# Kernel optimization log

Hardware: AMD Instinct MI355X
Metric: run time of the kernel (lower is better)

## Reference

```python
import jax, jax.numpy as jnp
import numpy as np


def _gcn_layer(x, W, b, src, dst, norm, n_nodes):
    # x: [N, Fin]; transform first (PyG GCNConv): h = x @ W
    h = x @ W  # [N, Fout]
    # gather-scale-scatter: out[d] += norm_e * h[s] over edges (incl. self loops)
    msgs = h[src] * norm[:, None]  # [E+N, Fout]
    agg = jax.ops.segment_sum(msgs, dst, num_segments=n_nodes)
    return agg + b


def setup_inputs() -> dict:
    key = jax.random.key(0)
    k1, k2, k3, k4 = jax.random.split(key, 4)
    N, E, F_IN, HID, OUT = 50000, 800000, 128, 256, 128
    x = jax.random.normal(k1, (N, F_IN), dtype=jnp.float32)
    edge_index = jax.random.randint(k2, (2, E), 0, N, dtype=jnp.int64)
    W1 = jax.random.normal(k3, (F_IN, HID), dtype=jnp.float32) / np.sqrt(F_IN)
    b1 = jnp.zeros((HID,), dtype=jnp.float32)
    W2 = jax.random.normal(k4, (HID, OUT), dtype=jnp.float32) / np.sqrt(HID)
    b2 = jnp.zeros((OUT,), dtype=jnp.float32)
    return {"x": x, "edge_index": edge_index, "W1": W1, "b1": b1, "W2": W2, "b2": b2}


def reference(x, edge_index, W1, b1, W2, b2):
    N = x.shape[0]
    # GCN normalization with self loops: A_hat = D^-1/2 (A + I) D^-1/2
    self_loops = jnp.arange(N, dtype=edge_index.dtype)
    src = jnp.concatenate([edge_index[0], self_loops])
    dst = jnp.concatenate([edge_index[1], self_loops])
    deg = jax.ops.segment_sum(jnp.ones_like(dst, dtype=x.dtype), dst, num_segments=N)
    dinv = jnp.where(deg > 0, jax.lax.rsqrt(deg), 0.0)
    norm = dinv[src] * dinv[dst]  # [E+N]
    h = _gcn_layer(x, W1, b1, src, dst, norm, N)
    h = jax.nn.relu(h)  # dropout is identity in eval mode
    out = _gcn_layer(h, W2, b2, src, dst, norm, N)
    return out  # unsupervised mode returns raw embeddings [N, 128]
```

## Files before the change

kernel.cpp:

```cpp
#include <hip/hip_runtime.h>
#include <hip/hip_bf16.h>


static constexpr int N_NODES = 50000;
static constexpr int N_EDGES = 800000;
static constexpr int F_IN = 128;
static constexpr int HID  = 256;
static constexpr int F_OUT = 128;

typedef __attribute__((ext_vector_type(8))) short short8;
typedef __attribute__((ext_vector_type(4))) float f32x4;

__device__ __forceinline__ unsigned short f2bf(float f) {
    union { float f; unsigned u; } x; x.f = f;
    unsigned r = x.u + 0x7FFF + ((x.u >> 16) & 1);
    return (unsigned short)(r >> 16);
}
__device__ __forceinline__ float bf2f(unsigned short h) {
    union { unsigned u; float f; } x; x.u = ((unsigned)h) << 16;
    return x.f;
}

__global__ void deg_pos_kernel(const int* __restrict__ dst, int* __restrict__ deg,
                               int* __restrict__ pos, int E) {
    int i = blockIdx.x * blockDim.x + threadIdx.x;
    if (i < E) pos[i] = atomicAdd(&deg[dst[i]], 1);
}

__global__ __launch_bounds__(256) void scan_reduce_dinv(const int* __restrict__ deg,
                                                        int* __restrict__ bsums,
                                                        float* __restrict__ dinv, int N) {
    int i = blockIdx.x * 256 + threadIdx.x;
    int v = (i < N) ? deg[i] : 0;
    if (i < N) dinv[i] = rsqrtf((float)(v + 1));
#pragma unroll
    for (int ofs = 32; ofs > 0; ofs >>= 1) v += __shfl_down(v, ofs);
    __shared__ int ws[4];
    if ((threadIdx.x & 63) == 0) ws[threadIdx.x >> 6] = v;
    __syncthreads();
    if (threadIdx.x == 0) bsums[blockIdx.x] = ws[0] + ws[1] + ws[2] + ws[3];
}

__global__ __launch_bounds__(256) void scan_final(const int* __restrict__ deg,
                                                  const int* __restrict__ bsums,
                                                  int* __restrict__ off, int N, int nb) {
    __shared__ int bs[256];
    __shared__ int s[256];
    const int tid = threadIdx.x;
    bs[tid] = (tid < nb) ? bsums[tid] : 0;
    const int i = blockIdx.x * 256 + tid;
    int v = (i < N) ? deg[i] : 0;
    s[tid] = v;
    __syncthreads();
    for (int ofs = 1; ofs < 256; ofs <<= 1) {
        int tb = (tid >= ofs) ? bs[tid - ofs] : 0;
        int tv = (tid >= ofs) ? s[tid - ofs] : 0;
        __syncthreads();
        bs[tid] += tb;
        s[tid] += tv;
        __syncthreads();
    }
    int bbase = (blockIdx.x == 0) ? 0 : bs[blockIdx.x - 1];
    int excl = (tid == 0) ? 0 : s[tid - 1];
    if (i <= N) off[i] = bbase + excl;
}

__global__ void scatter_kernel(const int* __restrict__ src, const int* __restrict__ dst,
                               const int* __restrict__ pos, const int* __restrict__ off,
                               int* __restrict__ csr, int E) {
    int i = blockIdx.x * blockDim.x + threadIdx.x;
    if (i < E) csr[off[dst[i]] + pos[i]] = src[i];
}

__global__ void prep_kernel(const float* __restrict__ x, const float* __restrict__ dinv,
                            unsigned short* __restrict__ xs,
                            const float* __restrict__ W1, unsigned short* __restrict__ w1t,
                            const float* __restrict__ W2, unsigned short* __restrict__ w2t,
                            int NBX, int NB1) {
    const int b = blockIdx.x;
    if (b < NBX) {
        int i = b * 256 + threadIdx.x;
        if (i < N_NODES * F_IN / 8) {
            float dv = dinv[i >> 4];
            float4 v0 = ((const float4*)x)[i * 2];
            float4 v1 = ((const float4*)x)[i * 2 + 1];
            short8 o;
            o[0] = (short)f2bf(v0.x * dv); o[1] = (short)f2bf(v0.y * dv);
            o[2] = (short)f2bf(v0.z * dv); o[3] = (short)f2bf(v0.w * dv);
            o[4] = (short)f2bf(v1.x * dv); o[5] = (short)f2bf(v1.y * dv);
            o[6] = (short)f2bf(v1.z * dv); o[7] = (short)f2bf(v1.w * dv);
            *(short8*)(xs + (size_t)i * 8) = o;
        }
    } else if (b < NBX + NB1) {
        int t = (b - NBX) * 256 + threadIdx.x;
        if (t < F_IN * HID) {
            int n = t / F_IN, k = t - n * F_IN;
            w1t[t] = f2bf(W1[(size_t)k * HID + n]);
        }
    } else {
        int t = (b - NBX - NB1) * 256 + threadIdx.x;
        if (t < HID * F_OUT) {
            int n = t / HID, k = t - n * HID;
            w2t[t] = f2bf(W2[(size_t)k * F_OUT + n]);
        }
    }
}

template <int MODE>
__global__ __launch_bounds__(256) void agg_bf16(const unsigned short* __restrict__ hs,
                                                const int* __restrict__ off,
                                                const int* __restrict__ csr,
                                                const float* __restrict__ dinv,
                                                const float* __restrict__ bias,
                                                void* __restrict__ outp, int N) {
    const int wid = threadIdx.x >> 6;
    const int n = blockIdx.x * 4 + wid;
    if (n >= N) return;
    const int lane = threadIdx.x & 63;
    const int lane16 = lane & 15;
    const int slot = lane >> 4;

    float va[8], vb[8], vc[8], vd[8];
#pragma unroll
    for (int j = 0; j < 8; j++) { va[j] = 0.f; vb[j] = 0.f; vc[j] = 0.f; vd[j] = 0.f; }

    if (slot == 0) {
        short8 s = *(const short8*)(hs + (size_t)n * 128 + lane16 * 8);
#pragma unroll
        for (int j = 0; j < 8; j++) va[j] = bf2f((unsigned short)s[j]);
    }

    const int e0 = off[n];
    const int e1 = off[n + 1];
    for (int e = e0 + slot; e < e1; e += 16) {
        const int i1 = e + 4, i2 = e + 8, i3 = e + 12;
        const float f1 = (i1 < e1) ? 1.f : 0.f;
        const float f2 = (i2 < e1) ? 1.f : 0.f;
        const float f3 = (i3 < e1) ? 1.f : 0.f;
        const int c1 = min(i1, e1 - 1), c2 = min(i2, e1 - 1), c3 = min(i3, e1 - 1);
        int s0 = csr[e];
        int s1 = csr[c1];
        int s2 = csr[c2];
        int s3 = csr[c3];
        short8 v0 = *(const short8*)(hs + (size_t)s0 * 128 + lane16 * 8);
        short8 v1 = *(const short8*)(hs + (size_t)s1 * 128 + lane16 * 8);
        short8 v2 = *(const short8*)(hs + (size_t)s2 * 128 + lane16 * 8);
        short8 v3 = *(const short8*)(hs + (size_t)s3 * 128 + lane16 * 8);
#pragma unroll
        for (int j = 0; j < 8; j++) va[j] += bf2f((unsigned short)v0[j]);
#pragma unroll
        for (int j = 0; j < 8; j++) vb[j] = fmaf(f1, bf2f((unsigned short)v1[j]), vb[j]);
#pragma unroll
        for (int j = 0; j < 8; j++) vc[j] = fmaf(f2, bf2f((unsigned short)v2[j]), vc[j]);
#pragma unroll
        for (int j = 0; j < 8; j++) vd[j] = fmaf(f3, bf2f((unsigned short)v3[j]), vd[j]);
    }
#pragma unroll
    for (int j = 0; j < 8; j++) va[j] += vb[j] + vc[j] + vd[j];

#pragma unroll
    for (int j = 0; j < 8; j++) va[j] += __shfl_down(va[j], 32);
#pragma unroll
    for (int j = 0; j < 8; j++) va[j] += __shfl_down(va[j], 16);

    if (lane < 16) {
        float dv = dinv[n];
        if (MODE == 0) {
            short8 o;
#pragma unroll
            for (int j = 0; j < 8; j++) o[j] = (short)f2bf(va[j] * dv);
            *(short8*)((unsigned short*)outp + (size_t)n * 128 + lane * 8) = o;
        } else {
            float* op = (float*)outp + (size_t)n * 128 + lane * 8;
            float4 o0, o1;
            o0.x = va[0] * dv + bias[lane * 8 + 0];
            o0.y = va[1] * dv + bias[lane * 8 + 1];
            o0.z = va[2] * dv + bias[lane * 8 + 2];
            o0.w = va[3] * dv + bias[lane * 8 + 3];
            o1.x = va[4] * dv + bias[lane * 8 + 4];
            o1.y = va[5] * dv + bias[lane * 8 + 5];
            o1.z = va[6] * dv + bias[lane * 8 + 6];
            o1.w = va[7] * dv + bias[lane * 8 + 7];
            ((float4*)op)[0] = o0;
            ((float4*)op)[1] = o1;
        }
    }
}

template <int K, int NC, int EPI>
__global__ __launch_bounds__(256) void mfma_gemm(const unsigned short* __restrict__ X,
                                                 const unsigned short* __restrict__ WT,
                                                 const float* __restrict__ bias,
                                                 const float* __restrict__ dinv,
                                                 unsigned short* __restrict__ out, int M) {
    constexpr int KC = K / 32;
    constexpr int TILES = NC / 32;
    const int wid = threadIdx.x >> 6;
    const int lane = threadIdx.x & 63;
    const int an = lane & 15;
    const int q = lane >> 4;
    const int rowgrp = wid & 1;
    const int colgrp = wid >> 1;
    const int m0 = blockIdx.x * 64 + rowgrp * 32;
    const int ntbase = colgrp * TILES;

    short8 a[2][KC];
#pragma unroll
    for (int r = 0; r < 2; r++) {
        int row = m0 + r * 16 + an;
        if (row >= M) row = M - 1;
        const unsigned short* xp = X + (size_t)row * K + q * 8;
#pragma unroll
        for (int c = 0; c < KC; c++) a[r][c] = *(const short8*)(xp + c * 32);
    }

    auto do_tile = [&](int t) {
        const int col = (ntbase + t) * 16 + an;
        const unsigned short* wp = WT + (size_t)col * K + q * 8;
        short8 b[KC];
#pragma unroll
        for (int c = 0; c < KC; c++) b[c] = *(const short8*)(wp + c * 32);
        f32x4 acc0 = {0.f, 0.f, 0.f, 0.f};
        f32x4 acc1 = {0.f, 0.f, 0.f, 0.f};
#pragma unroll
        for (int c = 0; c < KC; c++) {
            acc0 = __builtin_amdgcn_mfma_f32_16x16x32_bf16(a[0][c], b[c], acc0, 0, 0, 0);
            acc1 = __builtin_amdgcn_mfma_f32_16x16x32_bf16(a[1][c], b[c], acc1, 0, 0, 0);
        }
        float bv = (EPI == 1) ? bias[col] : 0.f;
#pragma unroll
        for (int rr = 0; rr < 4; rr++) {
            int m = m0 + q * 4 + rr;
            if (m < M) {
                float v = acc0[rr];
                if (EPI == 1) v = fmaxf(v + bv, 0.f);
                else v *= dinv[m];
                out[(size_t)m * NC + col] = f2bf(v);
            }
            int m2 = m0 + 16 + q * 4 + rr;
            if (m2 < M) {
                float v = acc1[rr];
                if (EPI == 1) v = fmaxf(v + bv, 0.f);
                else v *= dinv[m2];
                out[(size_t)m2 * NC + col] = f2bf(v);
            }
        }
    };

    if constexpr (K == 128) {
#pragma unroll 4
        for (int t = 0; t < TILES; t++) do_tile(t);
    } else {
#pragma unroll 2
        for (int t = 0; t < TILES; t++) do_tile(t);
    }
}

extern "C" void kernel_launch(void* const* d_in, const int* in_sizes, int n_in,
                              void* d_out, int out_size, void* d_ws, size_t ws_size,
                              hipStream_t stream) {
    const float* x  = (const float*)d_in[0];
    const int*   ei = (const int*)d_in[1];
    const float* W1 = (const float*)d_in[2];
    const float* b1 = (const float*)d_in[3];
    const float* W2 = (const float*)d_in[4];
    const float* b2 = (const float*)d_in[5];

    const int N = N_NODES;
    const int E = N_EDGES;
    const int* srcp = ei;
    const int* dstp = ei + E;

    char* base = (char*)d_ws;
    size_t o = 0;
    auto alloc = [&](size_t bytes) {
        void* p = base + o;
        o = (o + bytes + 255) & ~(size_t)255;
        return p;
    };
    int*            deg  = (int*)alloc((size_t)N * 4);
    int*            offs = (int*)alloc((size_t)(N + 1) * 4);
    float*          dinv = (float*)alloc((size_t)N * 4);
    int*            bsum = (int*)alloc(256 * 4);
    int*            pos  = (int*)alloc((size_t)E * 4);
    int*            csr  = (int*)alloc((size_t)E * 4);
    unsigned short* xs   = (unsigned short*)alloc((size_t)N * F_IN * 2);
    unsigned short* Y    = (unsigned short*)alloc((size_t)N * F_IN * 2);
    unsigned short* h2   = (unsigned short*)alloc((size_t)N * HID * 2);
    unsigned short* w1t  = (unsigned short*)alloc((size_t)F_IN * HID * 2);
    unsigned short* w2t  = (unsigned short*)alloc((size_t)HID * F_OUT * 2);
    unsigned short* hs2  = xs;

    hipMemsetAsync(deg, 0, (size_t)N * 4, stream);

    const int NB = (N + 256) / 256;
    const int NBX = (N * F_IN / 8 + 255) / 256;
    const int NB1 = (F_IN * HID + 255) / 256;
    const int NB2 = (HID * F_OUT + 255) / 256;

    deg_pos_kernel<<<(E + 255) / 256, 256, 0, stream>>>(dstp, deg, pos, E);
    scan_reduce_dinv<<<NB, 256, 0, stream>>>(deg, bsum, dinv, N);
    scan_final<<<NB, 256, 0, stream>>>(deg, bsum, offs, N, NB);
    scatter_kernel<<<(E + 255) / 256, 256, 0, stream>>>(srcp, dstp, pos, offs, csr, E);
    prep_kernel<<<NBX + NB1 + NB2, 256, 0, stream>>>(x, dinv, xs, W1, w1t, W2, w2t, NBX, NB1);

    agg_bf16<0><<<(N + 3) / 4, 256, 0, stream>>>(xs, offs, csr, dinv, nullptr, Y, N);
    mfma_gemm<F_IN, HID, 1><<<(N + 63) / 64, 256, 0, stream>>>(Y, w1t, b1, nullptr, h2, N);

    mfma_gemm<HID, F_OUT, 0><<<(N + 63) / 64, 256, 0, stream>>>(h2, w2t, nullptr, dinv, hs2, N);
    agg_bf16<1><<<(N + 3) / 4, 256, 0, stream>>>(hs2, offs, csr, dinv, b2, d_out, N);
}
```

Measured before the change: 263.6 us.

## Fuse both GEMMs via LDS-resident hidden tile and merge prep into other kernels

After: 251.6 us. -4.5%, faster.

```diff
diff --git a/kernel.cpp b/kernel.cpp
--- a/kernel.cpp
+++ b/kernel.cpp
@@ -7,6 +7,7 @@
 static constexpr int F_IN = 128;
 static constexpr int HID  = 256;
 static constexpr int F_OUT = 128;
+static constexpr int H2P  = HID + 8;
 
 typedef __attribute__((ext_vector_type(8))) short short8;
 typedef __attribute__((ext_vector_type(4))) float f32x4;
@@ -21,10 +22,28 @@
     return x.f;
 }
 
-__global__ void deg_pos_kernel(const int* __restrict__ dst, int* __restrict__ deg,
-                               int* __restrict__ pos, int E) {
-    int i = blockIdx.x * blockDim.x + threadIdx.x;
-    if (i < E) pos[i] = atomicAdd(&deg[dst[i]], 1);
+__global__ void deg_wt_kernel(const int* __restrict__ dst, int* __restrict__ deg,
+                              int* __restrict__ pos, int E,
+                              const float* __restrict__ W1, unsigned short* __restrict__ w1t,
+                              const float* __restrict__ W2, unsigned short* __restrict__ w2t,
+                              int EB, int NB1) {
+    const int b = blockIdx.x;
+    if (b < EB) {
+        int i = b * 256 + threadIdx.x;
+        if (i < E) pos[i] = atomicAdd(&deg[dst[i]], 1);
+    } else if (b < EB + NB1) {
+        int t = (b - EB) * 256 + threadIdx.x;
+        if (t < F_IN * HID) {
+            int n = t / F_IN, k = t - n * F_IN;
+            w1t[t] = f2bf(W1[(size_t)k * HID + n]);
+        }
+    } else {
+        int t = (b - EB - NB1) * 256 + threadIdx.x;
+        if (t < HID * F_OUT) {
+            int n = t / HID, k = t - n * HID;
+            w2t[t] = f2bf(W2[(size_t)k * F_OUT + n]);
+        }
+    }
 }
 
 __global__ __launch_bounds__(256) void scan_reduce_dinv(const int* __restrict__ deg,
@@ -41,12 +60,30 @@
     if (threadIdx.x == 0) bsums[blockIdx.x] = ws[0] + ws[1] + ws[2] + ws[3];
 }
 
-__global__ __launch_bounds__(256) void scan_final(const int* __restrict__ deg,
-                                                  const int* __restrict__ bsums,
-                                                  int* __restrict__ off, int N, int nb) {
+__global__ __launch_bounds__(256) void scan_final_scalex(const int* __restrict__ deg,
+                                                         const int* __restrict__ bsums,
+                                                         int* __restrict__ off, int N, int nb,
+                                                         const float* __restrict__ x,
+                                                         const float* __restrict__ dinv,
+                                                         unsigned short* __restrict__ xs) {
+    const int tid = threadIdx.x;
+    if ((int)blockIdx.x >= nb) {
+        int i = (blockIdx.x - nb) * 256 + tid;
+        if (i < N_NODES * F_IN / 8) {
+            float dv = dinv[i >> 4];
+            float4 v0 = ((const float4*)x)[i * 2];
+            float4 v1 = ((const float4*)x)[i * 2 + 1];
+            short8 o;
+            o[0] = (short)f2bf(v0.x * dv); o[1] = (short)f2bf(v0.y * dv);
+            o[2] = (short)f2bf(v0.z * dv); o[3] = (short)f2bf(v0.w * dv);
+            o[4] = (short)f2bf(v1.x * dv); o[5] = (short)f2bf(v1.y * dv);
+            o[6] = (short)f2bf(v1.z * dv); o[7] = (short)f2bf(v1.w * dv);
+            *(short8*)(xs + (size_t)i * 8) = o;
+        }
+        return;
+    }
     __shared__ int bs[256];
     __shared__ int s[256];
-    const int tid = threadIdx.x;
     bs[tid] = (tid < nb) ? bsums[tid] : 0;
     const int i = blockIdx.x * 256 + tid;
     int v = (i < N) ? deg[i] : 0;
@@ -70,40 +107,6 @@
                                int* __restrict__ csr, int E) {
     int i = blockIdx.x * blockDim.x + threadIdx.x;
     if (i < E) csr[off[dst[i]] + pos[i]] = src[i];
-}
-
-__global__ void prep_kernel(const float* __restrict__ x, const float* __restrict__ dinv,
-                            unsigned short* __restrict__ xs,
-                            const float* __restrict__ W1, unsigned short* __restrict__ w1t,
-                            const float* __restrict__ W2, unsigned short* __restrict__ w2t,
-                            int NBX, int NB1) {
-    const int b = blockIdx.x;
-    if (b < NBX) {
-        int i = b * 256 + threadIdx.x;
-        if (i < N_NODES * F_IN / 8) {
-            float dv = dinv[i >> 4];
-            float4 v0 = ((const float4*)x)[i * 2];
-            float4 v1 = ((const float4*)x)[i * 2 + 1];
-            short8 o;
-            o[0] = (short)f2bf(v0.x * dv); o[1] = (short)f2bf(v0.y * dv);
-            o[2] = (short)f2bf(v0.z * dv); o[3] = (short)f2bf(v0.w * dv);
-            o[4] = (short)f2bf(v1.x * dv); o[5] = (short)f2bf(v1.y * dv);
-            o[6] = (short)f2bf(v1.z * dv); o[7] = (short)f2bf(v1.w * dv);
-            *(short8*)(xs + (size_t)i * 8) = o;
-        }
-    } else if (b < NBX + NB1) {
-        int t = (b - NBX) * 256 + threadIdx.x;
-        if (t < F_IN * HID) {
-            int n = t / F_IN, k = t - n * F_IN;
-            w1t[t] = f2bf(W1[(size_t)k * HID + n]);
-        }
-    } else {
-        int t = (b - NBX - NB1) * 256 + threadIdx.x;
-        if (t < HID * F_OUT) {
-            int n = t / HID, k = t - n * HID;
-            w2t[t] = f2bf(W2[(size_t)k * F_OUT + n]);
-        }
-    }
 }
 
 template <int MODE>
@@ -187,14 +190,14 @@
     }
 }
 
-template <int K, int NC, int EPI>
-__global__ __launch_bounds__(256) void mfma_gemm(const unsigned short* __restrict__ X,
-                                                 const unsigned short* __restrict__ WT,
-                                                 const float* __restrict__ bias,
-                                                 const float* __restrict__ dinv,
-                                                 unsigned short* __restrict__ out, int M) {
-    constexpr int KC = K / 32;
-    constexpr int TILES = NC / 32;
+__global__ __launch_bounds__(256) void gemm12(const unsigned short* __restrict__ Y,
+                                              const unsigned short* __restrict__ w1t,
+                                              const float* __restrict__ b1,
+                                              const unsigned short* __restrict__ w2t,
+                                              const float* __restrict__ dinv,
+                                              unsigned short* __restrict__ hs2, int M) {
+    __shared__ unsigned short h2s[64 * H2P];
+
     const int wid = threadIdx.x >> 6;
     const int lane = threadIdx.x & 63;
     const int an = lane & 15;
@@ -202,57 +205,72 @@
     const int rowgrp = wid & 1;
     const int colgrp = wid >> 1;
     const int m0 = blockIdx.x * 64 + rowgrp * 32;
-    const int ntbase = colgrp * TILES;
-
-    short8 a[2][KC];
-#pragma unroll
-    for (int r = 0; r < 2; r++) {
-        int row = m0 + r * 16 + an;
-        if (row >= M) row = M - 1;
-        const unsigned short* xp = X + (size_t)row * K + q * 8;
-#pragma unroll
-        for (int c = 0; c < KC; c++) a[r][c] = *(const short8*)(xp + c * 32);
-    }
-
-    auto do_tile = [&](int t) {
-        const int col = (ntbase + t) * 16 + an;
-        const unsigned short* wp = WT + (size_t)col * K + q * 8;
-        short8 b[KC];
-#pragma unroll
-        for (int c = 0; c < KC; c++) b[c] = *(const short8*)(wp + c * 32);
-        f32x4 acc0 = {0.f, 0.f, 0.f, 0.f};
-        f32x4 acc1 = {0.f, 0.f, 0.f, 0.f};
-#pragma unroll
-        for (int c = 0; c < KC; c++) {
-            acc0 = __builtin_amdgcn_mfma_f32_16x16x32_bf16(a[0][c], b[c], acc0, 0, 0, 0);
-            acc1 = __builtin_amdgcn_mfma_f32_16x16x32_bf16(a[1][c], b[c], acc1, 0, 0, 0);
-        }
-        float bv = (EPI == 1) ? bias[col] : 0.f;
-#pragma unroll
-        for (int rr = 0; rr < 4; rr++) {
-            int m = m0 + q * 4 + rr;
-            if (m < M) {
-                float v = acc0[rr];
-                if (EPI == 1) v = fmaxf(v + bv, 0.f);
-                else v *= dinv[m];
-                out[(size_t)m * NC + col] = f2bf(v);
+    const int lrow0 = rowgrp * 32;
+
+    {
+        short8 a[2][4];
+#pragma unroll
+        for (int r = 0; r < 2; r++) {
+            int row = m0 + r * 16 + an;
+            if (row >= M) row = M - 1;
+            const unsigned short* xp = Y + (size_t)row * F_IN + q * 8;
+#pragma unroll
+            for (int c = 0; c < 4; c++) a[r][c] = *(const short8*)(xp + c * 32);
+        }
+#pragma unroll 4
+        for (int t = 0; t < 8; t++) {
+            const int col = (colgrp * 8 + t) * 16 + an;
+            const unsigned short* wp = w1t + (size_t)col * F_IN + q * 8;
+            short8 b[4];
+#pragma unroll
+            for (int c = 0; c < 4; c++) b[c] = *(const short8*)(wp + c * 32);
+            f32x4 acc0 = {0.f, 0.f, 0.f, 0.f};
+            f32x4 acc1 = {0.f, 0.f, 0.f, 0.f};
+#pragma unroll
+            for (int c = 0; c < 4; c++) {
+                acc0 = __builtin_amdgcn_mfma_f32_16x16x32_bf16(a[0][c], b[c], acc0, 0, 0, 0);
+                acc1 = __builtin_amdgcn_mfma_f32_16x16x32_bf16(a[1][c], b[c], acc1, 0, 0, 0);
             }
-            int m2 = m0 + 16 + q * 4 + rr;
-            if (m2 < M) {
-                float v = acc1[rr];
-                if (EPI == 1) v = fmaxf(v + bv, 0.f);
-                else v *= dinv[m2];
-                out[(size_t)m2 * NC + col] = f2bf(v);
+            const float bv = b1[col];
+#pragma unroll
+            for (int rr = 0; rr < 4; rr++) {
+                h2s[(lrow0 + q * 4 + rr) * H2P + col]      = f2bf(fmaxf(acc0[rr] + bv, 0.f));
+                h2s[(lrow0 + 16 + q * 4 + rr) * H2P + col] = f2bf(fmaxf(acc1[rr] + bv, 0.f));
             }
         }
-    };
-
-    if constexpr (K == 128) {
-#pragma unroll 4
-        for (int t = 0; t < TILES; t++) do_tile(t);
-    } else {
+    }
+    __syncthreads();
+
+    {
+        short8 a[2][8];
+#pragma unroll
+        for (int r = 0; r < 2; r++) {
+            const unsigned short* hp = &h2s[(lrow0 + r * 16 + an) * H2P + q * 8];
+#pragma unroll
+            for (int c = 0; c < 8; c++) a[r][c] = *(const short8*)(hp + c * 32);
+        }
 #pragma unroll 2
-        for (int t = 0; t < TILES; t++) do_tile(t);
+        for (int t = 0; t < 4; t++) {
+            const int col = (colgrp * 4 + t) * 16 + an;
+            const unsigned short* wp = w2t + (size_t)col * HID + q * 8;
+            short8 b[8];
+#pragma unroll
+            for (int c = 0; c < 8; c++) b[c] = *(const short8*)(wp + c * 32);
+            f32x4 acc0 = {0.f, 0.f, 0.f, 0.f};
+            f32x4 acc1 = {0.f, 0.f, 0.f, 0.f};
+#pragma unroll
+            for (int c = 0; c < 8; c++) {
+                acc0 = __builtin_amdgcn_mfma_f32_16x16x32_bf16(a[0][c], b[c], acc0, 0, 0, 0);
+                acc1 = __builtin_amdgcn_mfma_f32_16x16x32_bf16(a[1][c], b[c], acc1, 0, 0, 0);
+            }
+#pragma unroll
+            for (int rr = 0; rr < 4; rr++) {
+                int m = m0 + q * 4 + rr;
+                if (m < M) hs2[(size_t)m * F_OUT + col] = f2bf(acc0[rr] * dinv[m]);
+                int m2 = m0 + 16 + q * 4 + rr;
+                if (m2 < M) hs2[(size_t)m2 * F_OUT + col] = f2bf(acc1[rr] * dinv[m2]);
+            }
+        }
     }
 }
 
@@ -286,27 +304,24 @@
     int*            csr  = (int*)alloc((size_t)E * 4);
     unsigned short* xs   = (unsigned short*)alloc((size_t)N * F_IN * 2);
     unsigned short* Y    = (unsigned short*)alloc((size_t)N * F_IN * 2);
-    unsigned short* h2   = (unsigned short*)alloc((size_t)N * HID * 2);
     unsigned short* w1t  = (unsigned short*)alloc((size_t)F_IN * HID * 2);
     unsigned short* w2t  = (unsigned short*)alloc((size_t)HID * F_OUT * 2);
     unsigned short* hs2  = xs;
 
     hipMemsetAsync(deg, 0, (size_t)N * 4, stream);
 
-    const int NB = (N + 256) / 256;
+    const int NB  = (N + 256) / 256;
     const int NBX = (N * F_IN / 8 + 255) / 256;
+    const int EB  = (E + 255) / 256;
     const int NB1 = (F_IN * HID + 255) / 256;
     const int NB2 = (HID * F_OUT + 255) / 256;
 
-    deg_pos_kernel<<<(E + 255) / 256, 256, 0, stream>>>(dstp, deg, pos, E);
+    deg_wt_kernel<<<EB + NB1 + NB2, 256, 0, stream>>>(dstp, deg, pos, E, W1, w1t, W2, w2t, EB, NB1);
     scan_reduce_dinv<<<NB, 256, 0, stream>>>(deg, bsum, dinv, N);
-    scan_final<<<NB, 256, 0, stream>>>(deg, bsum, offs, N, NB);
-    scatter_kernel<<<(E + 255) / 256, 256, 0, stream>>>(srcp, dstp, pos, offs, csr, E);
-    prep_kernel<<<NBX + NB1 + NB2, 256, 0, stream>>>(x, dinv, xs, W1, w1t, W2, w2t, NBX, NB1);
+    scan_final_scalex<<<NB + NBX, 256, 0, stream>>>(deg, bsum, offs, N, NB, x, dinv, xs);
+    scatter_kernel<<<EB, 256, 0, stream>>>(srcp, dstp, pos, offs, csr, E);
 
     agg_bf16<0><<<(N + 3) / 4, 256, 0, stream>>>(xs, offs, csr, dinv, nullptr, Y, N);
-    mfma_gemm<F_IN, HID, 1><<<(N + 63) / 64, 256, 0, stream>>>(Y, w1t, b1, nullptr, h2, N);
-
-    mfma_gemm<HID, F_OUT, 0><<<(N + 63) / 64, 256, 0, stream>>>(h2, w2t, nullptr, dinv, hs2, N);
+    gemm12<<<(N + 63) / 64, 256, 0, stream>>>(Y, w1t, b1, w2t, dinv, hs2, N);
     agg_bf16<1><<<(N + 3) / 4, 256, 0, stream>>>(hs2, offs, csr, dinv, b2, d_out, N);
 }
```
